# Kernel tuning notes

Hardware: AMD Instinct MI355X
Metric: run time of the kernel (lower is better)

The kernel has to match this reference:

```python
import jax, jax.numpy as jnp
import numpy as np

N_NODES = 50000
HIDDEN = 128
N_EDGES = 600000
DROPOUT_RATE = 0.25


def setup_inputs() -> dict:
    key = jax.random.key(0)
    k_x, k_e, k_w1, k_w2 = jax.random.split(key, 4)
    x = jax.random.normal(k_x, (N_NODES, HIDDEN), dtype=jnp.float32)
    edge_index = jax.random.randint(k_e, (2, N_EDGES), 0, N_NODES, dtype=jnp.int64)
    # Linear layers: torch Linear default init ~ U(-1/sqrt(fan_in), 1/sqrt(fan_in))
    s = 1.0 / np.sqrt(HIDDEN)
    W1 = jax.random.uniform(k_w1, (HIDDEN, HIDDEN), jnp.float32, -s, s)
    b1 = jnp.zeros((HIDDEN,), jnp.float32)
    W2 = jax.random.uniform(k_w2, (HIDDEN, HIDDEN), jnp.float32, -s, s)
    b2 = jnp.zeros((HIDDEN,), jnp.float32)
    return {"x": x, "edge_index": edge_index, "W1": W1, "b1": b1, "W2": W2, "b2": b2}


def reference(x, edge_index, W1, b1, W2, b2):
    # Feature-dim dropout mask (bernoulli over hidden dim, broadcast over nodes).
    mask_key = jax.random.key(42)
    mask = jax.random.bernoulli(mask_key, 1.0 - DROPOUT_RATE, (x.shape[1],)).astype(x.dtype)
    xd = x * mask[None, :]  # [N, D]

    # GINConv aggregation: sum of source-node features at destination nodes.
    src, dst = edge_index[0], edge_index[1]
    agg = jax.ops.segment_sum(xd[src], dst, num_segments=x.shape[0])  # [N, D]

    # (1 + eps) * x + agg, eps = 0 (GINConv default)
    h = xd + agg

    # 2-layer MLP: Linear -> ReLU -> Linear
    h = jax.nn.relu(h @ W1 + b1)
    out = h @ W2 + b2
    return out
```

## Files before the change

kernel.cpp:

```cpp
#include <hip/hip_runtime.h>

#define N_NODES 50000
#define HIDDEN  128
#define N_EDGES 600000
#define BR      32
#define NB      ((N_NODES + 255) / 256)
#define NTILES  ((N_NODES + BR - 1) / BR)
#define E_PAD_MAX (N_EDGES + 3 * N_NODES)
#define SCSR_CAP 4096

typedef __attribute__((ext_vector_type(8))) short short8v;
typedef __attribute__((ext_vector_type(4))) float f32x4;

__device__ __forceinline__ unsigned rotl32(unsigned v, int r) {
  return (v << r) | (v >> (32 - r));
}

__device__ __forceinline__ void threefry2x32(unsigned x0, unsigned x1,
                                             unsigned& o0, unsigned& o1) {
  const unsigned ks0 = 0u, ks1 = 42u;
  const unsigned ks2 = ks0 ^ ks1 ^ 0x1BD11BDAu;
  const unsigned ks[3] = {ks0, ks1, ks2};
  const int rot[2][4] = {{13, 15, 26, 6}, {17, 29, 16, 24}};
  x0 += ks0; x1 += ks1;
#pragma unroll
  for (int i = 0; i < 5; ++i) {
#pragma unroll
    for (int j = 0; j < 4; ++j) {
      x0 += x1;
      x1 = rotl32(x1, rot[i & 1][j]);
      x1 ^= x0;
    }
    x0 += ks[(i + 1) % 3];
    x1 += ks[(i + 2) % 3] + (unsigned)(i + 1);
  }
  o0 = x0; o1 = x1;
}

__device__ __forceinline__ float col_mask(int c) {
  unsigned o0, o1;
  threefry2x32(0u, (unsigned)c, o0, o1);
  unsigned bits = o0 ^ o1;
  float u = __uint_as_float((bits >> 9) | 0x3f800000u) - 1.0f;
  return (u < 0.75f) ? 1.0f : 0.0f;
}

__device__ __forceinline__ unsigned short f2bf(float f) {
  unsigned u = __float_as_uint(f);
  u += 0x7fffu + ((u >> 16) & 1u);
  return (unsigned short)(u >> 16);
}

__device__ __forceinline__ float bflo(unsigned u) {
  return __uint_as_float(u << 16);
}
__device__ __forceinline__ float bfhi(unsigned u) {
  return __uint_as_float(u & 0xffff0000u);
}

__device__ __forceinline__ float rlane(float v, int l) {
  return __int_as_float(__builtin_amdgcn_readlane(__float_as_int(v), l));
}

__global__ __launch_bounds__(256) void prep_kernel(
    const float* __restrict__ x, const float* __restrict__ W1,
    const float* __restrict__ W2, const int* __restrict__ ei,
    unsigned short* __restrict__ xb, unsigned short* __restrict__ Wt1,
    unsigned short* __restrict__ Wt2, int* __restrict__ deg) {
  __shared__ float msk[HIDDEN];
  if (threadIdx.x < HIDDEN) msk[threadIdx.x] = col_mask(threadIdx.x);
  __syncthreads();

  const int gid = blockIdx.x * 256 + threadIdx.x;
  const int e0 = gid * 8;
  if (e0 < N_NODES * HIDDEN) {
    const int c0 = e0 & (HIDDEN - 1);
    const float4 v0 = *reinterpret_cast<const float4*>(x + e0);
    const float4 v1 = *reinterpret_cast<const float4*>(x + e0 + 4);
    unsigned short h[8];
    h[0] = f2bf(v0.x * msk[c0 + 0]);
    h[1] = f2bf(v0.y * msk[c0 + 1]);
    h[2] = f2bf(v0.z * msk[c0 + 2]);
    h[3] = f2bf(v0.w * msk[c0 + 3]);
    h[4] = f2bf(v1.x * msk[c0 + 4]);
    h[5] = f2bf(v1.y * msk[c0 + 5]);
    h[6] = f2bf(v1.z * msk[c0 + 6]);
    h[7] = f2bf(v1.w * msk[c0 + 7]);
    *reinterpret_cast<uint4*>(xb + e0) = *reinterpret_cast<uint4*>(h);
  }
  if (gid < N_EDGES) atomicAdd(deg + ei[N_EDGES + gid], 1);
  if (gid < HIDDEN * HIDDEN / 4) {
#pragma unroll
    for (int i = 0; i < 4; ++i) {
      int t = gid * 4 + i;
      int col = t >> 7, k = t & 127;
      Wt1[t] = f2bf(W1[k * HIDDEN + col]);
      Wt2[t] = f2bf(W2[k * HIDDEN + col]);
    }
  }
  if (gid < 16) {
    uint4 z; z.x = 0; z.y = 0; z.z = 0; z.w = 0;
    *reinterpret_cast<uint4*>(xb + (size_t)N_NODES * HIDDEN + gid * 8) = z;
  }
}

__global__ __launch_bounds__(256) void scanA_kernel(const int* __restrict__ deg,
                                                    int* __restrict__ bsum) {
  int idx = blockIdx.x * 256 + threadIdx.x;
  int v = (idx < N_NODES) ? ((deg[idx] + 3) & ~3) : 0;
#pragma unroll
  for (int off = 32; off; off >>= 1) v += __shfl_down(v, off, 64);
  __shared__ int ws4[4];
  if ((threadIdx.x & 63) == 0) ws4[threadIdx.x >> 6] = v;
  __syncthreads();
  if (threadIdx.x == 0) bsum[blockIdx.x] = ws4[0] + ws4[1] + ws4[2] + ws4[3];
}

__global__ __launch_bounds__(256) void scanB_kernel(const int* __restrict__ bsum,
                                                    int* __restrict__ bpre,
                                                    int* __restrict__ offs) {
  __shared__ int s[256];
  const int t = threadIdx.x;
  int v = (t < NB) ? bsum[t] : 0;
  s[t] = v;
  __syncthreads();
  int acc = v;
  for (int off = 1; off < 256; off <<= 1) {
    int add = (t >= off) ? s[t - off] : 0;
    __syncthreads();
    acc += add;
    s[t] = acc;
    __syncthreads();
  }
  if (t < NB) bpre[t] = acc - v;
  if (t == 0) offs[N_NODES] = s[255];
}

__global__ __launch_bounds__(256) void scanC_kernel(
    const int* __restrict__ deg, const int* __restrict__ bpre,
    int* __restrict__ offs, int* __restrict__ pos,
    unsigned short* __restrict__ csr) {
  __shared__ int s[256];
  const int t = threadIdx.x;
  const int idx = blockIdx.x * 256 + t;
  int d = (idx < N_NODES) ? deg[idx] : 0;
  int v = (d + 3) & ~3;
  s[t] = v;
  __syncthreads();
  int acc = v;
  for (int off = 1; off < 256; off <<= 1) {
    int add = (t >= off) ? s[t - off] : 0;
    __syncthreads();
    acc += add;
    s[t] = acc;
    __syncthreads();
  }
  if (idx < N_NODES) {
    int o = bpre[blockIdx.x] + acc - v;
    offs[idx] = o;
    pos[idx] = o;
    for (int w = o + d; w < o + v; ++w)
      csr[w] = (unsigned short)N_NODES;
  }
}

__global__ __launch_bounds__(256) void fill_kernel(const int* __restrict__ ei,
                                                   int* __restrict__ pos,
                                                   unsigned short* __restrict__ csr) {
  int e = blockIdx.x * blockDim.x + threadIdx.x;
  if (e >= N_EDGES) return;
  int src = ei[e];
  int dst = ei[N_EDGES + e];
  int p = atomicAdd(pos + dst, 1);
  csr[p] = (unsigned short)src;
}

template <bool LDSIDX>
__device__ __forceinline__ void gather2(
    int base, int wave, int q, int ql, int cs,
    const unsigned short* __restrict__ csr, const unsigned short* scsr,
    const int* loffs, const unsigned short* __restrict__ xb,
    unsigned short* H1) {
#pragma unroll
  for (int i = 0; i < 2; ++i) {
    const int row = wave * 8 + i * 4 + q;
    const int node = base + row;
    const bool valid = node < N_NODES;
    const int s = valid ? loffs[row] : 0;
    const int e = valid ? loffs[row + 1] : 0;
    const int on = valid ? node : N_NODES;
    const uint4 ov =
        *reinterpret_cast<const uint4*>(xb + (size_t)on * HIDDEN + ql * 8);
    float a0 = bflo(ov.x), a1 = bfhi(ov.x);
    float a2 = bflo(ov.y), a3 = bfhi(ov.y);
    float a4 = bflo(ov.z), a5 = bfhi(ov.z);
    float a6 = bflo(ov.w), a7 = bfhi(ov.w);

    uint2 pk; pk.x = 0; pk.y = 0;
    if (s < e) {
      pk = LDSIDX ? *reinterpret_cast<const uint2*>(scsr + (s - cs))
                  : *reinterpret_cast<const uint2*>(csr + s);
    }
    for (int j = s; j < e; j += 4) {
      const unsigned px = pk.x, py = pk.y;
      if (j + 4 < e) {
        pk = LDSIDX ? *reinterpret_cast<const uint2*>(scsr + (j + 4 - cs))
                    : *reinterpret_cast<const uint2*>(csr + j + 4);
      }
      const int i0 = (int)(px & 0xffffu), i1 = (int)(px >> 16);
      const int i2 = (int)(py & 0xffffu), i3 = (int)(py >> 16);
      const uint4 u0 =
          *reinterpret_cast<const uint4*>(xb + (size_t)i0 * HIDDEN + ql * 8);
      const uint4 u1 =
          *reinterpret_cast<const uint4*>(xb + (size_t)i1 * HIDDEN + ql * 8);
      const uint4 u2 =
          *reinterpret_cast<const uint4*>(xb + (size_t)i2 * HIDDEN + ql * 8);
      const uint4 u3 =
          *reinterpret_cast<const uint4*>(xb + (size_t)i3 * HIDDEN + ql * 8);
      a0 += bflo(u0.x) + bflo(u1.x) + bflo(u2.x) + bflo(u3.x);
      a1 += bfhi(u0.x) + bfhi(u1.x) + bfhi(u2.x) + bfhi(u3.x);
      a2 += bflo(u0.y) + bflo(u1.y) + bflo(u2.y) + bflo(u3.y);
      a3 += bfhi(u0.y) + bfhi(u1.y) + bfhi(u2.y) + bfhi(u3.y);
      a4 += bflo(u0.z) + bflo(u1.z) + bflo(u2.z) + bflo(u3.z);
      a5 += bfhi(u0.z) + bfhi(u1.z) + bfhi(u2.z) + bfhi(u3.z);
      a6 += bflo(u0.w) + bflo(u1.w) + bflo(u2.w) + bflo(u3.w);
      a7 += bfhi(u0.w) + bfhi(u1.w) + bfhi(u2.w) + bfhi(u3.w);
    }
    uint4 pw;
    pw.x = (unsigned)f2bf(a0) | ((unsigned)f2bf(a1) << 16);
    pw.y = (unsigned)f2bf(a2) | ((unsigned)f2bf(a3) << 16);
    pw.z = (unsigned)f2bf(a4) | ((unsigned)f2bf(a5) << 16);
    pw.w = (unsigned)f2bf(a6) | ((unsigned)f2bf(a7) << 16);
    const int byte = (row * 256 + ql * 16) ^ ((row & 7) << 4);
    *reinterpret_cast<uint4*>(reinterpret_cast<char*>(H1) + byte) = pw;
  }
}

__global__ __launch_bounds__(256) void fused_xb_kernel(
    const int* __restrict__ offs, const unsigned short* __restrict__ csr,
    const unsigned short* __restrict__ xb,
    const unsigned short* __restrict__ Wt1,
    const unsigned short* __restrict__ Wt2, const float* __restrict__ b1,
    const float* __restrict__ b2, float* __restrict__ out) {
  __shared__ unsigned short H1[BR * HIDDEN];
  __shared__ unsigned short H2[BR * HIDDEN];
  __shared__ unsigned short scsr[SCSR_CAP];
  __shared__ int loffs[BR + 1];

  const int tid = threadIdx.x;
  const int lane = tid & 63;
  const int wave = tid >> 6;
  const int base = blockIdx.x * BR;

  if (tid < BR + 1) {
    int idx = base + tid;
    loffs[tid] = offs[idx > N_NODES ? N_NODES : idx];
  }
  __syncthreads();
  const int cs = loffs[0];
  const int count = loffs[BR] - cs;
  const bool stage = (count <= SCSR_CAP);
  if (stage) {
    const unsigned* src = reinterpret_cast<const unsigned*>(csr + cs);
    unsigned* dst = reinterpret_cast<unsigned*>(scsr);
    for (int k = tid; k < (count >> 1); k += 256) dst[k] = src[k];
  }
  __syncthreads();

  const int q = lane >> 4;
  const int ql = lane & 15;

  if (stage)
    gather2<true>(base, wave, q, ql, cs, csr, scsr, loffs, xb, H1);
  else
    gather2<false>(base, wave, q, ql, cs, csr, scsr, loffs, xb, H1);
  __syncthreads();

  const int colbase = wave * 32;
  float bias1[2], bias2[2];
#pragma unroll
  for (int c = 0; c < 2; ++c) {
    bias1[c] = b1[colbase + c * 16 + (lane & 15)];
    bias2[c] = b2[colbase + c * 16 + (lane & 15)];
  }

  f32x4 acc[2][2] = {};
#pragma unroll
  for (int kt = 0; kt < 4; ++kt) {
    short8v a[2], b[2];
#pragma unroll
    for (int r = 0; r < 2; ++r) {
      int row = r * 16 + (lane & 15);
      int byte = (row * 256 + kt * 64 + (lane >> 4) * 16) ^ ((row & 7) << 4);
      a[r] = *reinterpret_cast<const short8v*>(
          reinterpret_cast<const char*>(H1) + byte);
    }
#pragma unroll
    for (int c = 0; c < 2; ++c) {
      int col = colbase + c * 16 + (lane & 15);
      b[c] = *reinterpret_cast<const short8v*>(
          reinterpret_cast<const char*>(Wt1) + col * 256 + kt * 64 +
          (lane >> 4) * 16);
    }
#pragma unroll
    for (int r = 0; r < 2; ++r)
#pragma unroll
      for (int c = 0; c < 2; ++c)
        acc[r][c] = __builtin_amdgcn_mfma_f32_16x16x32_bf16(a[r], b[c],
                                                            acc[r][c], 0, 0, 0);
  }
#pragma unroll
  for (int r = 0; r < 2; ++r)
#pragma unroll
    for (int c = 0; c < 2; ++c)
#pragma unroll
      for (int q2 = 0; q2 < 4; ++q2) {
        int row = r * 16 + (lane >> 4) * 4 + q2;
        int col = colbase + c * 16 + (lane & 15);
        float v = fmaxf(acc[r][c][q2] + bias1[c], 0.f);
        int byte = (row * 256 + col * 2) ^ ((row & 7) << 4);
        *reinterpret_cast<unsigned short*>(reinterpret_cast<char*>(H2) + byte) =
            f2bf(v);
      }
  __syncthreads();

  f32x4 acc2[2][2] = {};
#pragma unroll
  for (int kt = 0; kt < 4; ++kt) {
    short8v a[2], b[2];
#pragma unroll
    for (int r = 0; r < 2; ++r) {
      int row = r * 16 + (lane & 15);
      int byte = (row * 256 + kt * 64 + (lane >> 4) * 16) ^ ((row & 7) << 4);
      a[r] = *reinterpret_cast<const short8v*>(
          reinterpret_cast<const char*>(H2) + byte);
    }
#pragma unroll
    for (int c = 0; c < 2; ++c) {
      int col = colbase + c * 16 + (lane & 15);
      b[c] = *reinterpret_cast<const short8v*>(
          reinterpret_cast<const char*>(Wt2) + col * 256 + kt * 64 +
          (lane >> 4) * 16);
    }
#pragma unroll
    for (int r = 0; r < 2; ++r)
#pragma unroll
      for (int c = 0; c < 2; ++c)
        acc2[r][c] = __builtin_amdgcn_mfma_f32_16x16x32_bf16(
            a[r], b[c], acc2[r][c], 0, 0, 0);
  }
#pragma unroll
  for (int r = 0; r < 2; ++r)
#pragma unroll
    for (int c = 0; c < 2; ++c)
#pragma unroll
      for (int q2 = 0; q2 < 4; ++q2) {
        int row = base + r * 16 + (lane >> 4) * 4 + q2;
        if (row < N_NODES) {
          int col = colbase + c * 16 + (lane & 15);
          out[(size_t)row * HIDDEN + col] = acc2[r][c][q2] + bias2[c];
        }
      }
}

__global__ __launch_bounds__(256) void scatter_kernel(
    const int* __restrict__ ei, const float* __restrict__ x,
    float* __restrict__ agg) {
  long long gid = (long long)blockIdx.x * blockDim.x + threadIdx.x;
  int e = (int)(gid >> 5);
  if (e >= N_EDGES) return;
  int sub = ((int)gid & 31) * 4;
  int src = ei[e];
  int dst = ei[N_EDGES + e];
  const float4 v = *reinterpret_cast<const float4*>(x + src * HIDDEN + sub);
  float* p = agg + dst * HIDDEN + sub;
  atomicAdd(p + 0, v.x);
  atomicAdd(p + 1, v.y);
  atomicAdd(p + 2, v.z);
  atomicAdd(p + 3, v.w);
}

__global__ __launch_bounds__(512) void mlp_kernel(
    const float* __restrict__ x, float* __restrict__ io,
    const float* __restrict__ W1, const float* __restrict__ b1,
    const float* __restrict__ W2, const float* __restrict__ b2) {
  __shared__ float W1s[HIDDEN * HIDDEN];
  __shared__ float W2s[HIDDEN * HIDDEN];

  const int tid = threadIdx.x;
#pragma unroll
  for (int i = 0; i < 8; ++i) {
    int idx = (i * 512 + tid) * 4;
    *reinterpret_cast<float4*>(W1s + idx) =
        *reinterpret_cast<const float4*>(W1 + idx);
    *reinterpret_cast<float4*>(W2s + idx) =
        *reinterpret_cast<const float4*>(W2 + idx);
  }

  const int lane = tid & 63;
  const int wave = tid >> 6;
  const int c0 = 2 * lane, c1 = 2 * lane + 1;

  const float m0 = col_mask(c0);
  const float m1 = col_mask(c1);
  const float bb1x = b1[c0], bb1y = b1[c1];
  const float bb2x = b2[c0], bb2y = b2[c1];

  __syncthreads();

  const int gwave = blockIdx.x * 8 + wave;
  const int nwaves = gridDim.x * 8;

  for (int pr = gwave; pr < N_NODES / 2; pr += nwaves) {
    const int baseA = (2 * pr) * HIDDEN;
    const int baseB = baseA + HIDDEN;

    float2 xA = *reinterpret_cast<const float2*>(x + baseA + c0);
    float2 gA = *reinterpret_cast<const float2*>(io + baseA + c0);
    float2 xB = *reinterpret_cast<const float2*>(x + baseB + c0);
    float2 gB = *reinterpret_cast<const float2*>(io + baseB + c0);

    float hA0 = m0 * (xA.x + gA.x), hA1 = m1 * (xA.y + gA.y);
    float hB0 = m0 * (xB.x + gB.x), hB1 = m1 * (xB.y + gB.y);

    float aA0 = bb1x, aA1 = bb1y, aB0 = bb1x, aB1 = bb1y;
#pragma unroll
    for (int k = 0; k < HIDDEN; ++k) {
      const int sl = k >> 1;
      float hkA = (k & 1) ? rlane(hA1, sl) : rlane(hA0, sl);
      float hkB = (k & 1) ? rlane(hB1, sl) : rlane(hB0, sl);
      float2 w = *reinterpret_cast<const float2*>(W1s + k * HIDDEN + c0);
      aA0 = fmaf(hkA, w.x, aA0);
      aA1 = fmaf(hkA, w.y, aA1);
      aB0 = fmaf(hkB, w.x, aB0);
      aB1 = fmaf(hkB, w.y, aB1);
    }
    aA0 = fmaxf(aA0, 0.0f); aA1 = fmaxf(aA1, 0.0f);
    aB0 = fmaxf(aB0, 0.0f); aB1 = fmaxf(aB1, 0.0f);

    float oA0 = bb2x, oA1 = bb2y, oB0 = bb2x, oB1 = bb2y;
#pragma unroll
    for (int k = 0; k < HIDDEN; ++k) {
      const int sl = k >> 1;
      float hkA = (k & 1) ? rlane(aA1, sl) : rlane(aA0, sl);
      float hkB = (k & 1) ? rlane(aB1, sl) : rlane(aB0, sl);
      float2 w = *reinterpret_cast<const float2*>(W2s + k * HIDDEN + c0);
      oA0 = fmaf(hkA, w.x, oA0);
      oA1 = fmaf(hkA, w.y, oA1);
      oB0 = fmaf(hkB, w.x, oB0);
      oB1 = fmaf(hkB, w.y, oB1);
    }

    *reinterpret_cast<float2*>(io + baseA + c0) = make_float2(oA0, oA1);
    *reinterpret_cast<float2*>(io + baseB + c0) = make_float2(oB0, oB1);
  }
}

extern "C" void kernel_launch(void* const* d_in, const int* in_sizes, int n_in,
                              void* d_out, int out_size, void* d_ws,
                              size_t ws_size, hipStream_t stream) {
  (void)in_sizes; (void)n_in; (void)out_size;
  const float* x  = (const float*)d_in[0];
  const int*   ei = (const int*)d_in[1];
  const float* W1 = (const float*)d_in[2];
  const float* b1 = (const float*)d_in[3];
  const float* W2 = (const float*)d_in[4];
  const float* b2 = (const float*)d_in[5];
  float* out = (float*)d_out;

  const size_t int_bytes = (size_t)(N_NODES + (N_NODES + 1) + N_NODES + 2 * NB) * 4;
  const size_t int_pad   = (int_bytes + 15) & ~(size_t)15;
  const size_t csr_bytes = (size_t)E_PAD_MAX * 2;
  const size_t wt_bytes  = 2 * (size_t)HIDDEN * HIDDEN * 2;
  const size_t xb_bytes  = (size_t)(N_NODES + 1) * HIDDEN * 2;
  const size_t need = int_pad + csr_bytes + wt_bytes + xb_bytes;

  if (ws_size >= need) {
    char* wsb = (char*)d_ws;
    int* deg  = (int*)wsb;
    int* offs = deg + N_NODES;
    int* pos  = offs + N_NODES + 1;
    int* bsum = pos + N_NODES;
    int* bpre = bsum + NB;
    unsigned short* csr = (unsigned short*)(wsb + int_pad);
    unsigned short* Wt1 = (unsigned short*)(wsb + int_pad + csr_bytes);
    unsigned short* Wt2 = Wt1 + HIDDEN * HIDDEN;
    unsigned short* xb  = Wt2 + HIDDEN * HIDDEN;

    hipMemsetAsync(deg, 0, (size_t)N_NODES * 4, stream);
    const int nprep = (N_NODES * HIDDEN / 8 + 255) / 256;
    prep_kernel<<<nprep, 256, 0, stream>>>(x, W1, W2, ei, xb, Wt1, Wt2, deg);
    scanA_kernel<<<NB, 256, 0, stream>>>(deg, bsum);
    scanB_kernel<<<1, 256, 0, stream>>>(bsum, bpre, offs);
    scanC_kernel<<<NB, 256, 0, stream>>>(deg, bpre, offs, pos, csr);
    fill_kernel<<<(N_EDGES + 255) / 256, 256, 0, stream>>>(ei, pos, csr);
    fused_xb_kernel<<<NTILES, 256, 0, stream>>>(offs, csr, xb, Wt1, Wt2, b1,
                                                b2, out);
  } else {
    hipMemsetAsync(out, 0, (size_t)N_NODES * HIDDEN * sizeof(float), stream);
    const long long total = (long long)N_EDGES * 32;
    scatter_kernel<<<(int)((total + 255) / 256), 256, 0, stream>>>(ei, x, out);
    mlp_kernel<<<256, 512, 0, stream>>>(x, out, W1, b1, W2, b2);
  }
}
```

Measured before the change: 117.8 us.

## Merge three scan kernels into single-pass chained scan; prefetch gather rows

Replaces the three-kernel scan (block sums, single-block prefix, per-block scan) with one kernel. Each block waits on its predecessor's done flag and takes its running prefix, which removes two launches and their dependency gaps. The edge gather loop is changed to issue the next four neighbour-row loads before accumulating the current four, using the zero padding row as a dummy target. The gather loop over rows is no longer unrolled. The chained scan relies on blocks being scheduled in order, and the prefetch adds an extra dummy load per row and more register pressure.

```diff
diff --git a/kernel.cpp b/kernel.cpp
--- a/kernel.cpp
+++ b/kernel.cpp
@@ -104,24 +104,17 @@
   }
 }
 
-__global__ __launch_bounds__(256) void scanA_kernel(const int* __restrict__ deg,
-                                                    int* __restrict__ bsum) {
-  int idx = blockIdx.x * 256 + threadIdx.x;
-  int v = (idx < N_NODES) ? ((deg[idx] + 3) & ~3) : 0;
-#pragma unroll
-  for (int off = 32; off; off >>= 1) v += __shfl_down(v, off, 64);
-  __shared__ int ws4[4];
-  if ((threadIdx.x & 63) == 0) ws4[threadIdx.x >> 6] = v;
-  __syncthreads();
-  if (threadIdx.x == 0) bsum[blockIdx.x] = ws4[0] + ws4[1] + ws4[2] + ws4[3];
-}
-
-__global__ __launch_bounds__(256) void scanB_kernel(const int* __restrict__ bsum,
-                                                    int* __restrict__ bpre,
-                                                    int* __restrict__ offs) {
+__global__ __launch_bounds__(256) void scan_kernel(
+    const int* __restrict__ deg, int* __restrict__ offs,
+    int* __restrict__ pos, unsigned short* __restrict__ csr,
+    int* __restrict__ pref, int* __restrict__ done) {
   __shared__ int s[256];
+  __shared__ int sbase;
   const int t = threadIdx.x;
-  int v = (t < NB) ? bsum[t] : 0;
+  const int b = blockIdx.x;
+  const int idx = b * 256 + t;
+  const int d = (idx < N_NODES) ? deg[idx] : 0;
+  const int v = (d + 3) & ~3;
   s[t] = v;
   __syncthreads();
   int acc = v;
@@ -132,31 +125,22 @@
     s[t] = acc;
     __syncthreads();
   }
-  if (t < NB) bpre[t] = acc - v;
-  if (t == 0) offs[N_NODES] = s[255];
-}
-
-__global__ __launch_bounds__(256) void scanC_kernel(
-    const int* __restrict__ deg, const int* __restrict__ bpre,
-    int* __restrict__ offs, int* __restrict__ pos,
-    unsigned short* __restrict__ csr) {
-  __shared__ int s[256];
-  const int t = threadIdx.x;
-  const int idx = blockIdx.x * 256 + t;
-  int d = (idx < N_NODES) ? deg[idx] : 0;
-  int v = (d + 3) & ~3;
-  s[t] = v;
-  __syncthreads();
-  int acc = v;
-  for (int off = 1; off < 256; off <<= 1) {
-    int add = (t >= off) ? s[t - off] : 0;
-    __syncthreads();
-    acc += add;
-    s[t] = acc;
-    __syncthreads();
-  }
+  if (t == 255) {
+    int prev = 0;
+    if (b > 0) {
+      while (atomicAdd(&done[b - 1], 0) == 0) {
+      }
+      prev = atomicAdd(&pref[b - 1], 0);
+    }
+    pref[b] = prev + acc;
+    __threadfence();
+    atomicExch(&done[b], 1);
+    sbase = prev;
+    if (b == NB - 1) offs[N_NODES] = prev + acc;
+  }
+  __syncthreads();
   if (idx < N_NODES) {
-    int o = bpre[blockIdx.x] + acc - v;
+    const int o = sbase + acc - v;
     offs[idx] = o;
     pos[idx] = o;
     for (int w = o + d; w < o + v; ++w)
@@ -181,7 +165,7 @@
     const unsigned short* __restrict__ csr, const unsigned short* scsr,
     const int* loffs, const unsigned short* __restrict__ xb,
     unsigned short* H1) {
-#pragma unroll
+#pragma unroll 1
   for (int i = 0; i < 2; ++i) {
     const int row = wave * 8 + i * 4 + q;
     const int node = base + row;
@@ -196,35 +180,52 @@
     float a4 = bflo(ov.z), a5 = bfhi(ov.z);
     float a6 = bflo(ov.w), a7 = bfhi(ov.w);
 
-    uint2 pk; pk.x = 0; pk.y = 0;
-    if (s < e) {
+    const bool h0 = s < e;
+    uint2 pk;
+    pk.x = 0; pk.y = 0;
+    if (h0)
       pk = LDSIDX ? *reinterpret_cast<const uint2*>(scsr + (s - cs))
                   : *reinterpret_cast<const uint2*>(csr + s);
-    }
+    int i0 = h0 ? (int)(pk.x & 0xffffu) : N_NODES;
+    int i1 = h0 ? (int)(pk.x >> 16) : N_NODES;
+    int i2 = h0 ? (int)(pk.y & 0xffffu) : N_NODES;
+    int i3 = h0 ? (int)(pk.y >> 16) : N_NODES;
+    uint4 c0 = *reinterpret_cast<const uint4*>(xb + (size_t)i0 * HIDDEN + ql * 8);
+    uint4 c1 = *reinterpret_cast<const uint4*>(xb + (size_t)i1 * HIDDEN + ql * 8);
+    uint4 c2 = *reinterpret_cast<const uint4*>(xb + (size_t)i2 * HIDDEN + ql * 8);
+    uint4 c3 = *reinterpret_cast<const uint4*>(xb + (size_t)i3 * HIDDEN + ql * 8);
+
     for (int j = s; j < e; j += 4) {
-      const unsigned px = pk.x, py = pk.y;
-      if (j + 4 < e) {
-        pk = LDSIDX ? *reinterpret_cast<const uint2*>(scsr + (j + 4 - cs))
-                    : *reinterpret_cast<const uint2*>(csr + j + 4);
-      }
-      const int i0 = (int)(px & 0xffffu), i1 = (int)(px >> 16);
-      const int i2 = (int)(py & 0xffffu), i3 = (int)(py >> 16);
-      const uint4 u0 =
-          *reinterpret_cast<const uint4*>(xb + (size_t)i0 * HIDDEN + ql * 8);
-      const uint4 u1 =
-          *reinterpret_cast<const uint4*>(xb + (size_t)i1 * HIDDEN + ql * 8);
-      const uint4 u2 =
-          *reinterpret_cast<const uint4*>(xb + (size_t)i2 * HIDDEN + ql * 8);
-      const uint4 u3 =
-          *reinterpret_cast<const uint4*>(xb + (size_t)i3 * HIDDEN + ql * 8);
-      a0 += bflo(u0.x) + bflo(u1.x) + bflo(u2.x) + bflo(u3.x);
-      a1 += bfhi(u0.x) + bfhi(u1.x) + bfhi(u2.x) + bfhi(u3.x);
-      a2 += bflo(u0.y) + bflo(u1.y) + bflo(u2.y) + bflo(u3.y);
-      a3 += bfhi(u0.y) + bfhi(u1.y) + bfhi(u2.y) + bfhi(u3.y);
-      a4 += bflo(u0.z) + bflo(u1.z) + bflo(u2.z) + bflo(u3.z);
-      a5 += bfhi(u0.z) + bfhi(u1.z) + bfhi(u2.z) + bfhi(u3.z);
-      a6 += bflo(u0.w) + bflo(u1.w) + bflo(u2.w) + bflo(u3.w);
-      a7 += bfhi(u0.w) + bfhi(u1.w) + bfhi(u2.w) + bfhi(u3.w);
+      const int jn = j + 4;
+      const bool more = jn < e;
+      uint2 pk2;
+      pk2.x = 0; pk2.y = 0;
+      if (more)
+        pk2 = LDSIDX ? *reinterpret_cast<const uint2*>(scsr + (jn - cs))
+                     : *reinterpret_cast<const uint2*>(csr + jn);
+      const int n0 = more ? (int)(pk2.x & 0xffffu) : N_NODES;
+      const int n1 = more ? (int)(pk2.x >> 16) : N_NODES;
+      const int n2 = more ? (int)(pk2.y & 0xffffu) : N_NODES;
+      const int n3 = more ? (int)(pk2.y >> 16) : N_NODES;
+      const uint4 d0 =
+          *reinterpret_cast<const uint4*>(xb + (size_t)n0 * HIDDEN + ql * 8);
+      const uint4 d1 =
+          *reinterpret_cast<const uint4*>(xb + (size_t)n1 * HIDDEN + ql * 8);
+      const uint4 d2 =
+          *reinterpret_cast<const uint4*>(xb + (size_t)n2 * HIDDEN + ql * 8);
+      const uint4 d3 =
+          *reinterpret_cast<const uint4*>(xb + (size_t)n3 * HIDDEN + ql * 8);
+
+      a0 += bflo(c0.x) + bflo(c1.x) + bflo(c2.x) + bflo(c3.x);
+      a1 += bfhi(c0.x) + bfhi(c1.x) + bfhi(c2.x) + bfhi(c3.x);
+      a2 += bflo(c0.y) + bflo(c1.y) + bflo(c2.y) + bflo(c3.y);
+      a3 += bfhi(c0.y) + bfhi(c1.y) + bfhi(c2.y) + bfhi(c3.y);
+      a4 += bflo(c0.z) + bflo(c1.z) + bflo(c2.z) + bflo(c3.z);
+      a5 += bfhi(c0.z) + bfhi(c1.z) + bfhi(c2.z) + bfhi(c3.z);
+      a6 += bflo(c0.w) + bflo(c1.w) + bflo(c2.w) + bflo(c3.w);
+      a7 += bfhi(c0.w) + bfhi(c1.w) + bfhi(c2.w) + bfhi(c3.w);
+
+      c0 = d0; c1 = d1; c2 = d2; c3 = d3;
     }
     uint4 pw;
     pw.x = (unsigned)f2bf(a0) | ((unsigned)f2bf(a1) << 16);
@@ -244,7 +245,7 @@
     const float* __restrict__ b2, float* __restrict__ out) {
   __shared__ unsigned short H1[BR * HIDDEN];
   __shared__ unsigned short H2[BR * HIDDEN];
-  __shared__ unsigned short scsr[SCSR_CAP];
+  __shared__ __align__(16) unsigned short scsr[SCSR_CAP];
   __shared__ int loffs[BR + 1];
 
   const int tid = threadIdx.x;
@@ -468,8 +469,8 @@
   const float* b2 = (const float*)d_in[5];
   float* out = (float*)d_out;
 
-  const size_t int_bytes = (size_t)(N_NODES + (N_NODES + 1) + N_NODES + 2 * NB) * 4;
-  const size_t int_pad   = (int_bytes + 15) & ~(size_t)15;
+  const size_t int_words = (size_t)N_NODES + NB + (N_NODES + 1) + N_NODES + NB;
+  const size_t int_pad   = (int_words * 4 + 15) & ~(size_t)15;
   const size_t csr_bytes = (size_t)E_PAD_MAX * 2;
   const size_t wt_bytes  = 2 * (size_t)HIDDEN * HIDDEN * 2;
   const size_t xb_bytes  = (size_t)(N_NODES + 1) * HIDDEN * 2;
@@ -478,21 +479,19 @@
   if (ws_size >= need) {
     char* wsb = (char*)d_ws;
     int* deg  = (int*)wsb;
-    int* offs = deg + N_NODES;
+    int* done = deg + N_NODES;
+    int* offs = done + NB;
     int* pos  = offs + N_NODES + 1;
-    int* bsum = pos + N_NODES;
-    int* bpre = bsum + NB;
+    int* pref = pos + N_NODES;
     unsigned short* csr = (unsigned short*)(wsb + int_pad);
     unsigned short* Wt1 = (unsigned short*)(wsb + int_pad + csr_bytes);
     unsigned short* Wt2 = Wt1 + HIDDEN * HIDDEN;
     unsigned short* xb  = Wt2 + HIDDEN * HIDDEN;
 
-    hipMemsetAsync(deg, 0, (size_t)N_NODES * 4, stream);
+    hipMemsetAsync(deg, 0, (size_t)(N_NODES + NB) * 4, stream);
     const int nprep = (N_NODES * HIDDEN / 8 + 255) / 256;
     prep_kernel<<<nprep, 256, 0, stream>>>(x, W1, W2, ei, xb, Wt1, Wt2, deg);
-    scanA_kernel<<<NB, 256, 0, stream>>>(deg, bsum);
-    scanB_kernel<<<1, 256, 0, stream>>>(bsum, bpre, offs);
-    scanC_kernel<<<NB, 256, 0, stream>>>(deg, bpre, offs, pos, csr);
+    scan_kernel<<<NB, 256, 0, stream>>>(deg, offs, pos, csr, pref, done);
     fill_kernel<<<(N_EDGES + 255) / 256, 256, 0, stream>>>(ei, pos, csr);
     fused_xb_kernel<<<NTILES, 256, 0, stream>>>(offs, csr, xb, Wt1, Wt2, b1,
                                                 b2, out);
```

New measurement: 354.6 us. 3.01x slower.
